# Kernel optimization log

Measured on AMD Instinct MI355X. Metric: run time of the kernel, lower is better.

The kernel has to match this reference:

```python
import jax, jax.numpy as jnp
import numpy as np

N = 50000        # nodes
E = 800000       # edges (avg degree 16)
HID = 256        # hidden_size
HEADS = 8        # num_heads
HD = HID // HEADS  # head_dim = 32


def setup_inputs() -> dict:
    key = jax.random.key(0)
    ks = jax.random.split(key, 10)
    h = jax.random.normal(ks[0], (N, HID), dtype=jnp.float32)
    val = jax.random.uniform(ks[1], (E,), dtype=jnp.float32)
    Wq = jax.random.normal(ks[2], (HID, HID), dtype=jnp.float32) * 0.02
    Wk = jax.random.normal(ks[3], (HID, HID), dtype=jnp.float32) * 0.02
    Wv = jax.random.normal(ks[4], (HID, HID), dtype=jnp.float32) * 0.02
    bq = jnp.zeros((HID,), dtype=jnp.float32)
    bk = jnp.zeros((HID,), dtype=jnp.float32)
    bv = jnp.zeros((HID,), dtype=jnp.float32)
    # CSR rows expanded to per-edge row ids (sorted, like row_ptr expansion)
    edge_rows = jnp.sort(jax.random.randint(ks[5], (E,), 0, N, dtype=jnp.int32))
    col_ind = jax.random.randint(ks[6], (E,), 0, N, dtype=jnp.int32)
    return {"h": h, "val": val, "Wq": Wq, "bq": bq, "Wk": Wk, "bk": bk,
            "Wv": Wv, "bv": bv, "edge_rows": edge_rows, "col_ind": col_ind}


def reference(h, val, Wq, bq, Wk, bk, Wv, bv, edge_rows, col_ind):
    scaling = HD ** (-0.5)
    # projections; reshape splits hidden as (head_dim, heads) with heads fastest,
    # exactly as in the torch module: reshape(N, head_dim, num_heads)
    q = ((h @ Wq + bq).reshape(N, HD, HEADS)) * scaling
    k = (h @ Wk + bk).reshape(N, HD, HEADS)
    v = (h @ Wv + bv).reshape(N, HD, HEADS)

    # SDDMM restricted to edges: score[e, head] = <q[row_e], k[col_e]> * A.val[e]
    score = jnp.einsum('edh,edh->eh', q[edge_rows], k[col_ind]) * val[:, None]  # [E, HEADS]

    # per-destination-row softmax over incident edges (stable, segment ops)
    m = jax.ops.segment_max(score, edge_rows, num_segments=N)        # [N, HEADS]
    m = jnp.where(jnp.isfinite(m), m, jnp.zeros_like(m))             # empty rows
    e = jnp.exp(score - m[edge_rows])                                # [E, HEADS]
    denom = jax.ops.segment_sum(e, edge_rows, num_segments=N)        # [N, HEADS]
    attn = e / denom[edge_rows]

    # SpMM: out[i] = sum over edges (i, j) of attn * v[j]
    contrib = attn[:, None, :] * v[col_ind]                          # [E, HD, HEADS]
    out = jax.ops.segment_sum(contrib, edge_rows, num_segments=N)    # [N, HD, HEADS]
    return out.reshape(N, -1)                                        # [N, HID]
```

## Files before the change

kernel.cpp:

```cpp
#include <hip/hip_runtime.h>
#include <hip/hip_bf16.h>
#include <math.h>

static constexpr int kN   = 50000;
static constexpr int kE   = 800000;
static constexpr int kHID = 256;
static constexpr int kHD  = 32;

typedef short bf16x8 __attribute__((ext_vector_type(8)));
typedef float f32x4  __attribute__((ext_vector_type(4)));
typedef unsigned short us8 __attribute__((ext_vector_type(8)));

__device__ __forceinline__ float b2f(unsigned short u) {
  union { unsigned v; float f; } c; c.v = ((unsigned)u) << 16; return c.f;
}

__device__ __forceinline__ unsigned short f2bu(float f) {
  __hip_bfloat16 b = __float2bfloat16(f);
  union { __hip_bfloat16 b; unsigned short u; } c; c.b = b; return c.u;
}

__device__ __forceinline__ void load_lds16(const void* g, void* l) {
  __builtin_amdgcn_global_load_lds(
      (const __attribute__((address_space(1))) unsigned int*)(unsigned long long)(uintptr_t)g,
      (__attribute__((address_space(3))) unsigned int*)(unsigned int)(uintptr_t)l,
      16, 0, 0);
}

__global__ void split_h_kernel(const float* __restrict__ h,
                               __hip_bfloat16* __restrict__ Ah) {
  int idx = blockIdx.x * 256 + threadIdx.x;
  Ah[idx] = __float2bfloat16(h[idx]);
}

__global__ void build_bt_kernel(const float* __restrict__ Wq, const float* __restrict__ bq,
                                const float* __restrict__ Wk, const float* __restrict__ bk,
                                const float* __restrict__ Wv, const float* __restrict__ bv,
                                __hip_bfloat16* __restrict__ Bt, float* __restrict__ biasP) {
  const int n  = blockIdx.x;
  const int kk = threadIdx.x;
  const int g  = n >> 8;
  const int cc = n & 255;
  const int c  = ((cc & 31) << 3) + (cc >> 5);
  const float scale = (g == 0) ? 0.17677669529663689f : 1.0f;
  const float* W = (g == 0) ? Wq : ((g == 1) ? Wk : Wv);
  Bt[n * 256 + kk] = __float2bfloat16(W[kk * 256 + c] * scale);
  if (kk == 0) {
    const float* b = (g == 0) ? bq : ((g == 1) ? bk : bv);
    biasP[n] = b[c] * scale;
  }
}

__global__ void build_row_ptr(const int* __restrict__ er, int* __restrict__ rp) {
  int i = blockIdx.x * blockDim.x + threadIdx.x;
  if (i > kN) return;
  int lo = 0, hi = kE;
  while (lo < hi) {
    int mid = (lo + hi) >> 1;
    if (er[mid] < i) lo = mid + 1; else hi = mid;
  }
  rp[i] = lo;
}

__global__ __launch_bounds__(256) void gemm_qkv_kernel(
    const __hip_bfloat16* __restrict__ Ah,
    const __hip_bfloat16* __restrict__ Bt, const float* __restrict__ biasP,
    __hip_bfloat16* __restrict__ qb, __hip_bfloat16* __restrict__ kvb) {
  __shared__ __align__(16) char smemRaw[34816];
  short* smemA = (short*)smemRaw;
  short* smemB = (short*)(smemRaw + 16384);
  short* smemC = (short*)smemRaw;

  const int L   = blockIdx.x;
  const int xcd = L & 7;
  const int t   = L >> 3;
  const int nt  = t % 6;
  const int mg  = t / 6;
  const int mt  = mg * 8 + xcd;
  if (mt >= 391) return;
  const int colBase = nt * 128;
  const int rowBase = mt * 128;

  const int tid  = threadIdx.x;
  const int wave = tid >> 6;
  const int lane = tid & 63;
  const int wm = wave & 1;
  const int wn = wave >> 1;

  f32x4 acc[4][4];
#pragma unroll
  for (int i = 0; i < 4; ++i)
#pragma unroll
    for (int j = 0; j < 4; ++j) acc[i][j] = f32x4{0.f, 0.f, 0.f, 0.f};

  for (int k0 = 0; k0 < 256; k0 += 64) {
    __syncthreads();
#pragma unroll
    for (int j = 0; j < 4; ++j) {
      int s = (wave * 4 + j) * 64 + lane;
      int r = s >> 3, cp = s & 7;
      int c = cp ^ (r & 7);
      int grow = rowBase + r;
      grow = grow < kN ? grow : kN - 1;
      const char* gp = (const char*)Ah + (size_t)grow * 512 + k0 * 2 + c * 16;
      load_lds16(gp, (char*)smemA + (wave * 4 + j) * 1024);
    }
#pragma unroll
    for (int j = 0; j < 4; ++j) {
      int s = (wave * 4 + j) * 64 + lane;
      int r = s >> 3, cp = s & 7;
      int c = cp ^ (r & 7);
      const char* gp = (const char*)Bt + (size_t)(colBase + r) * 512 + k0 * 2 + c * 16;
      load_lds16(gp, (char*)smemB + (wave * 4 + j) * 1024);
    }
    __syncthreads();

    const int rq = lane & 15, qd = lane >> 4;
#pragma unroll
    for (int ks = 0; ks < 2; ++ks) {
      bf16x8 af[4], bfr[4];
#pragma unroll
      for (int mi = 0; mi < 4; ++mi) {
        int r = wm * 64 + mi * 16 + rq;
        int c = (ks * 4 + qd) ^ (r & 7);
        af[mi] = *(const bf16x8*)&smemA[r * 64 + c * 8];
      }
#pragma unroll
      for (int nj = 0; nj < 4; ++nj) {
        int r = wn * 64 + nj * 16 + rq;
        int c = (ks * 4 + qd) ^ (r & 7);
        bfr[nj] = *(const bf16x8*)&smemB[r * 64 + c * 8];
      }
#pragma unroll
      for (int mi = 0; mi < 4; ++mi)
#pragma unroll
        for (int nj = 0; nj < 4; ++nj)
          acc[mi][nj] = __builtin_amdgcn_mfma_f32_16x16x32_bf16(
              af[mi], bfr[nj], acc[mi][nj], 0, 0, 0);
    }
  }

  __syncthreads();
#pragma unroll
  for (int nj = 0; nj < 4; ++nj) {
    const int cl = wn * 64 + nj * 16 + (lane & 15);
    const float bb = biasP[colBase + cl];
#pragma unroll
    for (int mi = 0; mi < 4; ++mi) {
      const int rl = wm * 64 + mi * 16 + (lane >> 4) * 4;
#pragma unroll
      for (int reg = 0; reg < 4; ++reg) {
        smemC[(rl + reg) * 136 + cl] = (short)f2bu(acc[mi][nj][reg] + bb);
      }
    }
  }
  __syncthreads();

  const int g = colBase >> 8;
#pragma unroll
  for (int it = 0; it < 8; ++it) {
    const int r   = it * 16 + (tid >> 4);
    const int c16 = tid & 15;
    const int row = rowBase + r;
    if (row < kN) {
      bf16x8 vls = *(const bf16x8*)&smemC[r * 136 + c16 * 8];
      const int cc = (colBase & 255) + c16 * 8;
      __hip_bfloat16* dst =
          (g == 0) ? (qb + (size_t)row * 256 + cc)
                   : (kvb + (size_t)row * 512 + (g == 2 ? 256 : 0) + cc);
      *(bf16x8*)dst = vls;
    }
  }
}

__global__ __launch_bounds__(256) void edge_attn_kernel(
    const __hip_bfloat16* __restrict__ qb, const __hip_bfloat16* __restrict__ kvb,
    const int* __restrict__ row_ptr, const int* __restrict__ col_ind,
    const float* __restrict__ val, float* __restrict__ out) {
  const int wave = threadIdx.x >> 6;
  const int lane = threadIdx.x & 63;
  const int half = lane >> 5;
  const int sl   = lane & 31;
  const int row = blockIdx.x * 4 + wave;
  if (row >= kN) return;

  const int e0 = row_ptr[row];
  const int e1 = row_ptr[row + 1];

  const us8 qu = *(const us8*)(qb + (size_t)row * 256 + sl * 8);
  float qf[8];
#pragma unroll
  for (int j = 0; j < 8; ++j) qf[j] = b2f(qu[j]);

  float denom = 0.f;
  float acc[8];
#pragma unroll
  for (int j = 0; j < 8; ++j) acc[j] = 0.f;

  if (e0 < e1) {
    us8 kS[4], vS[4];
    float wS[4];
    const int elast = e1 - 1;
#pragma unroll
    for (int j = 0; j < 4; ++j) {
      const int eh = min(e0 + 2 * j + half, elast);
      const int c = col_ind[eh];
      wS[j] = val[eh];
      kS[j] = *(const us8*)(kvb + (size_t)c * 512 + sl * 8);
      vS[j] = *(const us8*)(kvb + (size_t)c * 512 + 256 + sl * 8);
    }

    for (int e = e0; e < e1; e += 8) {
#pragma unroll
      for (int j = 0; j < 4; ++j) {
        const us8 kc = kS[j], vc = vS[j];
        const float wc = wS[j];
        {
          const int ehN = min(e + 8 + 2 * j + half, elast);
          const int c = col_ind[ehN];
          wS[j] = val[ehN];
          kS[j] = *(const us8*)(kvb + (size_t)c * 512 + sl * 8);
          vS[j] = *(const us8*)(kvb + (size_t)c * 512 + 256 + sl * 8);
        }

        float s = 0.f;
#pragma unroll
        for (int jj = 0; jj < 8; ++jj) s = fmaf(qf[jj], b2f(kc[jj]), s);
        s += __shfl_xor(s, 1);
        s += __shfl_xor(s, 2);
        s *= wc;

        float p = __expf(s);
        p = ((e + 2 * j + half) < e1) ? p : 0.f;
        denom += p;
#pragma unroll
        for (int jj = 0; jj < 8; ++jj) acc[jj] = fmaf(p, b2f(vc[jj]), acc[jj]);
      }
    }
  }

#pragma unroll
  for (int j = 0; j < 8; ++j) acc[j] += __shfl_xor(acc[j], 32);
  denom += __shfl_xor(denom, 32);

  const float inv = (denom > 0.f) ? (1.0f / denom) : 0.f;
  const int h = sl >> 2;
  const int dbase = (sl & 3) * 8 + half * 4;
  float* o = out + (size_t)row * 256 + h;
#pragma unroll
  for (int jj = 0; jj < 4; ++jj)
    o[(dbase + jj) * 8] = acc[half * 4 + jj] * inv;
}

extern "C" void kernel_launch(void* const* d_in, const int* in_sizes, int n_in,
                              void* d_out, int out_size, void* d_ws, size_t ws_size,
                              hipStream_t stream) {
  const float* h   = (const float*)d_in[0];
  const float* val = (const float*)d_in[1];
  const float* Wq  = (const float*)d_in[2];
  const float* bq  = (const float*)d_in[3];
  const float* Wk  = (const float*)d_in[4];
  const float* bk  = (const float*)d_in[5];
  const float* Wv  = (const float*)d_in[6];
  const float* bv  = (const float*)d_in[7];
  const int* edge_rows = (const int*)d_in[8];
  const int* col_ind   = (const int*)d_in[9];
  float* out = (float*)d_out;

  char* ws = (char*)d_ws;
  __hip_bfloat16* Ah  = (__hip_bfloat16*)ws;                 ws += (size_t)kN * 256 * 2;
  __hip_bfloat16* Bt  = (__hip_bfloat16*)ws;                 ws += (size_t)768 * 256 * 2;
  float*          biasP = (float*)ws;                        ws += 768 * 4;
  __hip_bfloat16* qb  = (__hip_bfloat16*)ws;                 ws += (size_t)kN * 256 * 2;
  __hip_bfloat16* kvb = (__hip_bfloat16*)ws;                 ws += (size_t)kN * 512 * 2;
  int* row_ptr = (int*)ws;

  split_h_kernel<<<kN, 256, 0, stream>>>(h, Ah);
  build_bt_kernel<<<768, 256, 0, stream>>>(Wq, bq, Wk, bk, Wv, bv, Bt, biasP);
  build_row_ptr<<<(kN + 1 + 255) / 256, 256, 0, stream>>>(edge_rows, row_ptr);

  gemm_qkv_kernel<<<8 * 6 * 49, 256, 0, stream>>>(Ah, Bt, biasP, qb, kvb);

  edge_attn_kernel<<<(kN + 3) / 4, 256, 0, stream>>>(qb, kvb, row_ptr, col_ind,
                                                     val, out);
}
```

Before: 288.5 us.

## Deepen index prefetch in edge attention, use DPP reductions and exp2, vectorize cast

The edge attention loop now prefetches col_ind and val two groups ahead, while the K/V gathers stay one group ahead, so index-load latency no longer sits on the gather path. The quad reductions use DPP moves instead of shuffles, and q is prescaled by log2(e) so the kernel can call exp2f. The fp32-to-bf16 cast of h now handles 8 elements per thread with vector loads and stores. In exchange the edge kernel uses more registers and runs a 16-edge main loop, which adds masked padding work for low-degree rows.

```diff
diff --git a/kernel.cpp b/kernel.cpp
--- a/kernel.cpp
+++ b/kernel.cpp
@@ -18,6 +18,19 @@
 __device__ __forceinline__ unsigned short f2bu(float f) {
   __hip_bfloat16 b = __float2bfloat16(f);
   union { __hip_bfloat16 b; unsigned short u; } c; c.b = b; return c.u;
+}
+
+__device__ __forceinline__ float quad_add_xor1(float s) {
+  union { float f; int i; } a, b;
+  a.f = s;
+  b.i = __builtin_amdgcn_mov_dpp(a.i, 0xB1, 0xF, 0xF, true);
+  return s + b.f;
+}
+__device__ __forceinline__ float quad_add_xor2(float s) {
+  union { float f; int i; } a, b;
+  a.f = s;
+  b.i = __builtin_amdgcn_mov_dpp(a.i, 0x4E, 0xF, 0xF, true);
+  return s + b.f;
 }
 
 __device__ __forceinline__ void load_lds16(const void* g, void* l) {
@@ -30,7 +43,12 @@
 __global__ void split_h_kernel(const float* __restrict__ h,
                                __hip_bfloat16* __restrict__ Ah) {
   int idx = blockIdx.x * 256 + threadIdx.x;
-  Ah[idx] = __float2bfloat16(h[idx]);
+  const f32x4* hp = (const f32x4*)(h + (size_t)idx * 8);
+  f32x4 a = hp[0], b = hp[1];
+  us8 o;
+  o[0] = f2bu(a[0]); o[1] = f2bu(a[1]); o[2] = f2bu(a[2]); o[3] = f2bu(a[3]);
+  o[4] = f2bu(b[0]); o[5] = f2bu(b[1]); o[6] = f2bu(b[2]); o[7] = f2bu(b[3]);
+  *(us8*)(Ah + (size_t)idx * 8) = o;
 }
 
 __global__ void build_bt_kernel(const float* __restrict__ Wq, const float* __restrict__ bq,
@@ -190,7 +208,7 @@
   const us8 qu = *(const us8*)(qb + (size_t)row * 256 + sl * 8);
   float qf[8];
 #pragma unroll
-  for (int j = 0; j < 8; ++j) qf[j] = b2f(qu[j]);
+  for (int j = 0; j < 8; ++j) qf[j] = b2f(qu[j]) * 1.4426950408889634f;
 
   float denom = 0.f;
   float acc[8];
@@ -198,45 +216,72 @@
   for (int j = 0; j < 8; ++j) acc[j] = 0.f;
 
   if (e0 < e1) {
+    const char* kvbL = (const char*)kvb + sl * 16;
+    const int elast = e1 - 1;
+
     us8 kS[4], vS[4];
     float wS[4];
-    const int elast = e1 - 1;
-#pragma unroll
-    for (int j = 0; j < 4; ++j) {
-      const int eh = min(e0 + 2 * j + half, elast);
-      const int c = col_ind[eh];
-      wS[j] = val[eh];
-      kS[j] = *(const us8*)(kvb + (size_t)c * 512 + sl * 8);
-      vS[j] = *(const us8*)(kvb + (size_t)c * 512 + 256 + sl * 8);
-    }
-
-    for (int e = e0; e < e1; e += 8) {
-#pragma unroll
-      for (int j = 0; j < 4; ++j) {
-        const us8 kc = kS[j], vc = vS[j];
-        const float wc = wS[j];
-        {
-          const int ehN = min(e + 8 + 2 * j + half, elast);
-          const int c = col_ind[ehN];
-          wS[j] = val[ehN];
-          kS[j] = *(const us8*)(kvb + (size_t)c * 512 + sl * 8);
-          vS[j] = *(const us8*)(kvb + (size_t)c * 512 + 256 + sl * 8);
-        }
-
-        float s = 0.f;
-#pragma unroll
-        for (int jj = 0; jj < 8; ++jj) s = fmaf(qf[jj], b2f(kc[jj]), s);
-        s += __shfl_xor(s, 1);
-        s += __shfl_xor(s, 2);
-        s *= wc;
-
-        float p = __expf(s);
-        p = ((e + 2 * j + half) < e1) ? p : 0.f;
-        denom += p;
-#pragma unroll
-        for (int jj = 0; jj < 8; ++jj) acc[jj] = fmaf(p, b2f(vc[jj]), acc[jj]);
-      }
-    }
+    int   colA[4], colB[4];
+    float valA[4], valB[4];
+
+    int c0[4]; float w0[4];
+#pragma unroll
+    for (int j = 0; j < 4; ++j) {
+      const int ea = min(e0 + 2 * j + half, elast);
+      c0[j] = col_ind[ea]; w0[j] = val[ea];
+    }
+#pragma unroll
+    for (int j = 0; j < 4; ++j) {
+      const int eb = min(e0 + 8 + 2 * j + half, elast);
+      colA[j] = col_ind[eb]; valA[j] = val[eb];
+    }
+#pragma unroll
+    for (int j = 0; j < 4; ++j) {
+      const int ec = min(e0 + 16 + 2 * j + half, elast);
+      colB[j] = col_ind[ec]; valB[j] = val[ec];
+    }
+#pragma unroll
+    for (int j = 0; j < 4; ++j) {
+      const size_t off = (size_t)c0[j] * 1024;
+      kS[j] = *(const us8*)(kvbL + off);
+      vS[j] = *(const us8*)(kvbL + off + 512);
+      wS[j] = w0[j];
+    }
+
+#define ATTN_GROUP(EB, CB, VB)                                            \
+    _Pragma("unroll")                                                     \
+    for (int j = 0; j < 4; ++j) {                                         \
+      const us8 kc = kS[j], vc = vS[j];                                   \
+      const float wc = wS[j];                                             \
+      {                                                                   \
+        const size_t off = (size_t)CB[j] * 1024;                          \
+        kS[j] = *(const us8*)(kvbL + off);                                \
+        vS[j] = *(const us8*)(kvbL + off + 512);                          \
+        wS[j] = VB[j];                                                    \
+      }                                                                   \
+      {                                                                   \
+        const int en = min((EB) + 24 + 2 * j + half, elast);              \
+        CB[j] = col_ind[en];                                              \
+        VB[j] = val[en];                                                  \
+      }                                                                   \
+      float s = 0.f;                                                      \
+      _Pragma("unroll")                                                   \
+      for (int jj = 0; jj < 8; ++jj) s = fmaf(qf[jj], b2f(kc[jj]), s);    \
+      s = quad_add_xor1(s);                                               \
+      s = quad_add_xor2(s);                \
+      s *= wc;                                                            \
+      float p = exp2f(s);                                                 \
+      p = (((EB) + 2 * j + half) < e1) ? p : 0.f;                         \
+      denom += p;                                                         \
+      _Pragma("unroll")                                                   \
+      for (int jj = 0; jj < 8; ++jj) acc[jj] = fmaf(p, b2f(vc[jj]), acc[jj]); \
+    }
+
+    for (int e = e0; e < e1; e += 16) {
+      ATTN_GROUP(e, colA, valA);
+      ATTN_GROUP(e + 8, colB, valB);
+    }
+#undef ATTN_GROUP
   }
 
 #pragma unroll
@@ -275,7 +320,7 @@
   __hip_bfloat16* kvb = (__hip_bfloat16*)ws;                 ws += (size_t)kN * 512 * 2;
   int* row_ptr = (int*)ws;
 
-  split_h_kernel<<<kN, 256, 0, stream>>>(h, Ah);
+  split_h_kernel<<<kN / 8, 256, 0, stream>>>(h, Ah);
   build_bt_kernel<<<768, 256, 0, stream>>>(Wq, bq, Wk, bk, Wv, bv, Bt, biasP);
   build_row_ptr<<<(kN + 1 + 255) / 256, 256, 0, stream>>>(edge_rows, row_ptr);
 
```

Result: faster. 270.5 us (-6.2%).
